# Performance work log

Hardware: AMD Instinct MI355X
Metric: run time of the kernel (lower is better)

Reference implementation:

```python
import jax, jax.numpy as jnp
import numpy as np

NUM_HEADS = 16
EMBED_DIM = 1024

def setup_inputs() -> dict:
    key = jax.random.key(0)
    k1, k2, k3 = jax.random.split(key, 3)
    x = jax.random.normal(k1, (4, 2048, EMBED_DIM), dtype=jnp.float32)
    # Linear weights (lecun-style scaling for numerical sanity)
    w_qkv = jax.random.normal(k2, (EMBED_DIM, 3 * EMBED_DIM), dtype=jnp.float32) / np.sqrt(EMBED_DIM)
    w_out = jax.random.normal(k3, (EMBED_DIM, EMBED_DIM), dtype=jnp.float32) / np.sqrt(EMBED_DIM)
    return {"x": x, "w_qkv": w_qkv, "w_out": w_out}

def reference(x, w_qkv, w_out):
    b, s, d = x.shape
    h = NUM_HEADS
    dh = d // h
    qkv = x @ w_qkv                        # [b, s, 3d]
    q, k, v = jnp.split(qkv, 3, axis=-1)   # each [b, s, d]
    def split_heads(t):
        return t.reshape(b, s, h, dh).transpose(0, 2, 1, 3)  # [b, h, s, dh]
    q, k, v = split_heads(q), split_heads(k), split_heads(v)
    logits = jnp.einsum('bhsd,bhtd->bhst', q, k) / jnp.sqrt(jnp.asarray(dh, q.dtype))
    weights = jax.nn.softmax(logits, axis=-1)
    out = jnp.einsum('bhst,bhtd->bhsd', weights, v)
    out = out.transpose(0, 2, 1, 3).reshape(b, s, d)  # [b, s, d]
    return out @ w_out
```

## Files before the change

### kernel.cpp

```cpp
#include <hip/hip_runtime.h>
#include <hip/hip_bf16.h>
#include <math.h>

typedef unsigned short u16;
typedef unsigned long long u64;
typedef __attribute__((ext_vector_type(8))) short short8;
typedef __attribute__((ext_vector_type(4))) float floatx4;

#define BB 4
#define SS 2048
#define DD 1024
#define HH 16
#define DHH 64
#define BSZ (BB*SS)

__device__ inline u16 bf1(float f) {
  return (u16)((__float_as_uint(f) + 0x8000u) >> 16);
}
__device__ inline unsigned pk2bf(float a, float b) {
  return __builtin_amdgcn_perm(__float_as_uint(b) + 0x8000u,
                               __float_as_uint(a) + 0x8000u, 0x07060302u);
}

__device__ inline short8 ld16(const u16* p) {
  union { uint4 u; short8 s; } cv;
  cv.u = *(const uint4*)p;
  return cv.s;
}

__device__ inline void gload_lds16(const u16* g, u16* l) {
  __builtin_amdgcn_global_load_lds(
      (const __attribute__((address_space(1))) void*)g,
      (__attribute__((address_space(3))) void*)l, 16, 0, 0);
}

__global__ __launch_bounds__(256) void cvt_f32_bf16(
    const float* __restrict__ in, u16* __restrict__ out) {
  int t = blockIdx.x * 256 + threadIdx.x;
  const float4* p = (const float4*)in + (size_t)t * 2;
  float4 a = p[0], b = p[1];
  uint4 r;
  r.x = pk2bf(a.x, a.y); r.y = pk2bf(a.z, a.w);
  r.z = pk2bf(b.x, b.y); r.w = pk2bf(b.z, b.w);
  *((uint4*)out + t) = r;
}

__global__ __launch_bounds__(256) void transpose_f32_bf16(
    const float* __restrict__ in, u16* __restrict__ out, int K, int N) {
  __shared__ u16 tile[32][33];
  int k0 = blockIdx.y * 32, n0 = blockIdx.x * 32;
  int tx = threadIdx.x, ty = threadIdx.y;
  #pragma unroll
  for (int i = 0; i < 32; i += 8)
    tile[ty + i][tx] = bf1(in[(size_t)(k0 + ty + i) * N + n0 + tx]);
  __syncthreads();
  #pragma unroll
  for (int i = 0; i < 32; i += 8)
    out[(size_t)(n0 + ty + i) * K + k0 + tx] = tile[tx][ty + i];
}

template <int MODE>
__global__ __launch_bounds__(256) void gemm_nt(
    const u16* __restrict__ A, const u16* __restrict__ Bt,
    int M, int N, int K,
    float* __restrict__ outf, u16* __restrict__ q, u16* __restrict__ kk,
    u16* __restrict__ vv) {
  __shared__ __attribute__((aligned(16))) u16 As[128 * 32];
  __shared__ __attribute__((aligned(16))) u16 Bs[128 * 32];
  const int tid = threadIdx.x;
  const int lane = tid & 63;
  const int wave = tid >> 6;
  const int col = lane & 15, quad = lane >> 4;
  const int m0 = blockIdx.y * 128, n0 = blockIdx.x * 128;
  const int wm = (wave & 1) * 64, wn = (wave >> 1) * 64;

  floatx4 acc[4][4];
  #pragma unroll
  for (int i = 0; i < 4; i++)
    #pragma unroll
    for (int j = 0; j < 4; j++) acc[i][j] = (floatx4){0.f, 0.f, 0.f, 0.f};

  const u16* ga0 = A + (size_t)(m0 + (tid >> 2)) * K + (tid & 3) * 8;
  const u16* ga1 = ga0 + (size_t)64 * K;
  const u16* gb0 = Bt + (size_t)(n0 + (tid >> 2)) * K + (tid & 3) * 8;
  const u16* gb1 = gb0 + (size_t)64 * K;
  u16* lA0 = As + wave * 512;
  u16* lB0 = Bs + wave * 512;

  for (int kb = 0; kb < K; kb += 32) {
    __syncthreads();
    gload_lds16(ga0 + kb, lA0);
    gload_lds16(ga1 + kb, lA0 + 2048);
    gload_lds16(gb0 + kb, lB0);
    gload_lds16(gb1 + kb, lB0 + 2048);
    __syncthreads();
    short8 af[4], bfr[4];
    #pragma unroll
    for (int i = 0; i < 4; i++)
      af[i] = ld16(As + (wm + i * 16 + col) * 32 + quad * 8);
    #pragma unroll
    for (int i = 0; i < 4; i++)
      bfr[i] = ld16(Bs + (wn + i * 16 + col) * 32 + quad * 8);
    #pragma unroll
    for (int i = 0; i < 4; i++)
      #pragma unroll
      for (int j = 0; j < 4; j++)
        acc[i][j] = __builtin_amdgcn_mfma_f32_16x16x32_bf16(af[i], bfr[j],
                                                            acc[i][j], 0, 0, 0);
  }

  #pragma unroll
  for (int i = 0; i < 4; i++) {
    #pragma unroll
    for (int j = 0; j < 4; j++) {
      int gm0 = m0 + wm + i * 16 + quad * 4;
      int gn = n0 + wn + j * 16 + col;
      if (MODE == 0) {
        #pragma unroll
        for (int r = 0; r < 4; r++)
          outf[(size_t)(gm0 + r) * N + gn] = acc[i][j][r];
      } else {
        int which = gn >> 10;
        if (which == 2) {
          int dh = gn & 63, hh = (gn >> 6) & 15;
          int bb = gm0 >> 11, s = gm0 & 2047;
          uint2 pk;
          pk.x = pk2bf(acc[i][j][0], acc[i][j][1]);
          pk.y = pk2bf(acc[i][j][2], acc[i][j][3]);
          *(uint2*)(vv + ((size_t)((bb * HH + hh) * 64 + dh)) * SS + s) = pk;
        } else {
          int f = gn & 1023;
          u16* dst = (which == 0) ? q : kk;
          float sc = (which == 0) ? 0.18033688f : 1.0f;
          #pragma unroll
          for (int r = 0; r < 4; r++)
            dst[(size_t)(gm0 + r) * DD + f] = bf1(acc[i][j][r] * sc);
        }
      }
    }
  }
}

__global__ __launch_bounds__(256) void attn_kernel(
    const u16* __restrict__ Q, const u16* __restrict__ K,
    const u16* __restrict__ VT, u16* __restrict__ O) {
  __shared__ __attribute__((aligned(16))) u16 Ks[64 * 72];
  __shared__ __attribute__((aligned(16))) u16 Vs[80 * 72];
  __shared__ __attribute__((aligned(16))) u16 Ps[4][32 * 72];

  const int tid = threadIdx.x, lane = tid & 63, wave = tid >> 6;
  const int col = lane & 15, quad = lane >> 4;
  const int idx = blockIdx.x;
  const int qt = idx & 15;
  const int h = (idx >> 4) & 15;
  const int b = idx >> 8;

  const size_t rowbase = (size_t)b * SS;
  const int qrow0 = qt * 128 + wave * 32;

  short8 qf[2][2];
  #pragma unroll
  for (int qs = 0; qs < 2; qs++)
    #pragma unroll
    for (int kc = 0; kc < 2; kc++)
      qf[qs][kc] = ld16(Q + (rowbase + qrow0 + qs * 16 + col) * DD + h * DHH +
                        kc * 32 + quad * 8);

  const u16* kg = K + rowbase * DD + h * DHH;
  const u16* vg = VT + (size_t)(b * HH + h) * DHH * SS;

  {
    int r = 64 + (tid >> 4), c = (tid & 15) * 4;
    u16 val = (r == 64) ? (u16)0x3F80 : (u16)0;
    Vs[r * 72 + c] = val; Vs[r * 72 + c + 1] = val;
    Vs[r * 72 + c + 2] = val; Vs[r * 72 + c + 3] = val;
  }

  floatx4 o[2][5];
  #pragma unroll
  for (int qs = 0; qs < 2; qs++)
    #pragma unroll
    for (int mt = 0; mt < 5; mt++) o[qs][mt] = (floatx4){0.f, 0.f, 0.f, 0.f};

  const int srow = tid >> 2, sc = (tid & 3) * 16;
  u16* pw = &Ps[wave][0];

  for (int kt = 0; kt < SS; kt += 64) {
    uint4 k0 = *(const uint4*)(kg + (size_t)(kt + srow) * DD + sc);
    uint4 k1 = *(const uint4*)(kg + (size_t)(kt + srow) * DD + sc + 8);
    uint4 v0 = *(const uint4*)(vg + (size_t)srow * SS + kt + sc);
    uint4 v1 = *(const uint4*)(vg + (size_t)srow * SS + kt + sc + 8);
    __syncthreads();
    *(uint4*)(Ks + srow * 72 + sc) = k0;
    *(uint4*)(Ks + srow * 72 + sc + 8) = k1;
    *(uint4*)(Vs + srow * 72 + sc) = v0;
    *(uint4*)(Vs + srow * 72 + sc + 8) = v1;
    __syncthreads();

    #pragma unroll
    for (int qs = 0; qs < 2; qs++) {
      #pragma unroll
      for (int mt = 0; mt < 4; mt++) {
        floatx4 s = (floatx4){0.f, 0.f, 0.f, 0.f};
        s = __builtin_amdgcn_mfma_f32_16x16x32_bf16(
            ld16(Ks + (mt * 16 + col) * 72 + quad * 8), qf[qs][0], s, 0, 0, 0);
        s = __builtin_amdgcn_mfma_f32_16x16x32_bf16(
            ld16(Ks + (mt * 16 + col) * 72 + 32 + quad * 8), qf[qs][1], s, 0, 0, 0);
        uint2 pk;
        pk.x = pk2bf(__builtin_amdgcn_exp2f(s[0]), __builtin_amdgcn_exp2f(s[1]));
        pk.y = pk2bf(__builtin_amdgcn_exp2f(s[2]), __builtin_amdgcn_exp2f(s[3]));
        *(uint2*)(pw + (qs * 16 + col) * 72 + mt * 16 + quad * 4) = pk;
      }
    }

    #pragma unroll
    for (int qs = 0; qs < 2; qs++) {
      #pragma unroll
      for (int mt = 0; mt < 5; mt++) {
        #pragma unroll
        for (int kc = 0; kc < 2; kc++) {
          short8 a = ld16(Vs + (mt * 16 + col) * 72 + kc * 32 + quad * 8);
          short8 bb = ld16(pw + (qs * 16 + col) * 72 + kc * 32 + quad * 8);
          o[qs][mt] =
              __builtin_amdgcn_mfma_f32_16x16x32_bf16(a, bb, o[qs][mt], 0, 0, 0);
        }
      }
    }
  }

  #pragma unroll
  for (int qs = 0; qs < 2; qs++) {
    float l = __shfl(o[qs][4][0], col, 64);
    float inv = 1.0f / l;
    u16* ob = O + (rowbase + qrow0 + qs * 16 + col) * DD + h * DHH;
    #pragma unroll
    for (int mt = 0; mt < 4; mt++) {
      uint2 pk;
      pk.x = pk2bf(o[qs][mt][0] * inv, o[qs][mt][1] * inv);
      pk.y = pk2bf(o[qs][mt][2] * inv, o[qs][mt][3] * inv);
      *(uint2*)(ob + mt * 16 + quad * 4) = pk;
    }
  }
}

extern "C" void kernel_launch(void* const* d_in, const int* in_sizes, int n_in,
                              void* d_out, int out_size, void* d_ws,
                              size_t ws_size, hipStream_t stream) {
  const float* x = (const float*)d_in[0];
  const float* w_qkv = (const float*)d_in[1];
  const float* w_out = (const float*)d_in[2];
  float* out = (float*)d_out;

  u16* ws = (u16*)d_ws;
  u16* wT = ws;
  u16* q = wT + (size_t)3072 * 1024;
  u16* vt = q + (size_t)BSZ * DD;
  u16* k = (u16*)d_out;
  u16* xb = k + (size_t)BSZ * DD;
  u16* att = q;

  cvt_f32_bf16<<<dim3(BSZ * DD / (256 * 8)), 256, 0, stream>>>(x, xb);
  transpose_f32_bf16<<<dim3(3072 / 32, 1024 / 32), dim3(32, 8), 0, stream>>>(
      w_qkv, wT, 1024, 3072);
  gemm_nt<1><<<dim3(3072 / 128, BSZ / 128), 256, 0, stream>>>(
      xb, wT, BSZ, 3072, 1024, nullptr, q, k, vt);
  transpose_f32_bf16<<<dim3(1024 / 32, 1024 / 32), dim3(32, 8), 0, stream>>>(
      w_out, wT, 1024, 1024);
  attn_kernel<<<dim3(BB * HH * (SS / 128)), 256, 0, stream>>>(q, k, vt, att);
  gemm_nt<0><<<dim3(1024 / 128, BSZ / 128), 256, 0, stream>>>(
      att, wT, BSZ, 1024, 1024, out, nullptr, nullptr, nullptr);
}
```

Measured before the change: 306.0 us.

## Prefetch next K/V tile into registers and hoist LDS fragment loads in attention

The attention kernel now issues global loads for the next K/V tile right after the shared-memory store, so load latency overlaps the current tile's MFMA work. Loop order is swapped so each K and V fragment is read from LDS once and reused across both query sub-tiles, and P fragments are loaded up front. Block indexing is remapped so consecutive blocks handle different batch-heads of the same query tile, and launch bounds request 4 blocks per CU. The prefetch raises register pressure, and the last iteration makes one wasted wrapped-around load.

```diff
diff --git a/kernel.cpp b/kernel.cpp
--- a/kernel.cpp
+++ b/kernel.cpp
@@ -141,7 +141,7 @@
   }
 }
 
-__global__ __launch_bounds__(256) void attn_kernel(
+__global__ __launch_bounds__(256, 4) void attn_kernel(
     const u16* __restrict__ Q, const u16* __restrict__ K,
     const u16* __restrict__ VT, u16* __restrict__ O) {
   __shared__ __attribute__((aligned(16))) u16 Ks[64 * 72];
@@ -151,9 +151,10 @@
   const int tid = threadIdx.x, lane = tid & 63, wave = tid >> 6;
   const int col = lane & 15, quad = lane >> 4;
   const int idx = blockIdx.x;
-  const int qt = idx & 15;
-  const int h = (idx >> 4) & 15;
-  const int b = idx >> 8;
+  const int qt = idx >> 6;
+  const int bh = idx & 63;
+  const int h = bh & 15;
+  const int b = bh >> 4;
 
   const size_t rowbase = (size_t)b * SS;
   const int qrow0 = qt * 128 + wave * 32;
@@ -167,7 +168,7 @@
                         kc * 32 + quad * 8);
 
   const u16* kg = K + rowbase * DD + h * DHH;
-  const u16* vg = VT + (size_t)(b * HH + h) * DHH * SS;
+  const u16* vg = VT + (size_t)bh * DHH * SS;
 
   {
     int r = 64 + (tid >> 4), c = (tid & 15) * 4;
@@ -185,11 +186,12 @@
   const int srow = tid >> 2, sc = (tid & 3) * 16;
   u16* pw = &Ps[wave][0];
 
+  uint4 k0 = *(const uint4*)(kg + (size_t)srow * DD + sc);
+  uint4 k1 = *(const uint4*)(kg + (size_t)srow * DD + sc + 8);
+  uint4 v0 = *(const uint4*)(vg + (size_t)srow * SS + sc);
+  uint4 v1 = *(const uint4*)(vg + (size_t)srow * SS + sc + 8);
+
   for (int kt = 0; kt < SS; kt += 64) {
-    uint4 k0 = *(const uint4*)(kg + (size_t)(kt + srow) * DD + sc);
-    uint4 k1 = *(const uint4*)(kg + (size_t)(kt + srow) * DD + sc + 8);
-    uint4 v0 = *(const uint4*)(vg + (size_t)srow * SS + kt + sc);
-    uint4 v1 = *(const uint4*)(vg + (size_t)srow * SS + kt + sc + 8);
     __syncthreads();
     *(uint4*)(Ks + srow * 72 + sc) = k0;
     *(uint4*)(Ks + srow * 72 + sc + 8) = k1;
@@ -197,15 +199,23 @@
     *(uint4*)(Vs + srow * 72 + sc + 8) = v1;
     __syncthreads();
 
-    #pragma unroll
-    for (int qs = 0; qs < 2; qs++) {
-      #pragma unroll
-      for (int mt = 0; mt < 4; mt++) {
+    {
+      int nt_ = (kt + 64) & (SS - 1);
+      k0 = *(const uint4*)(kg + (size_t)(nt_ + srow) * DD + sc);
+      k1 = *(const uint4*)(kg + (size_t)(nt_ + srow) * DD + sc + 8);
+      v0 = *(const uint4*)(vg + (size_t)srow * SS + nt_ + sc);
+      v1 = *(const uint4*)(vg + (size_t)srow * SS + nt_ + sc + 8);
+    }
+
+    #pragma unroll
+    for (int mt = 0; mt < 4; mt++) {
+      short8 kf0 = ld16(Ks + (mt * 16 + col) * 72 + quad * 8);
+      short8 kf1 = ld16(Ks + (mt * 16 + col) * 72 + 32 + quad * 8);
+      #pragma unroll
+      for (int qs = 0; qs < 2; qs++) {
         floatx4 s = (floatx4){0.f, 0.f, 0.f, 0.f};
-        s = __builtin_amdgcn_mfma_f32_16x16x32_bf16(
-            ld16(Ks + (mt * 16 + col) * 72 + quad * 8), qf[qs][0], s, 0, 0, 0);
-        s = __builtin_amdgcn_mfma_f32_16x16x32_bf16(
-            ld16(Ks + (mt * 16 + col) * 72 + 32 + quad * 8), qf[qs][1], s, 0, 0, 0);
+        s = __builtin_amdgcn_mfma_f32_16x16x32_bf16(kf0, qf[qs][0], s, 0, 0, 0);
+        s = __builtin_amdgcn_mfma_f32_16x16x32_bf16(kf1, qf[qs][1], s, 0, 0, 0);
         uint2 pk;
         pk.x = pk2bf(__builtin_amdgcn_exp2f(s[0]), __builtin_amdgcn_exp2f(s[1]));
         pk.y = pk2bf(__builtin_amdgcn_exp2f(s[2]), __builtin_amdgcn_exp2f(s[3]));
@@ -213,17 +223,22 @@
       }
     }
 
-    #pragma unroll
-    for (int qs = 0; qs < 2; qs++) {
-      #pragma unroll
-      for (int mt = 0; mt < 5; mt++) {
-        #pragma unroll
-        for (int kc = 0; kc < 2; kc++) {
-          short8 a = ld16(Vs + (mt * 16 + col) * 72 + kc * 32 + quad * 8);
-          short8 bb = ld16(pw + (qs * 16 + col) * 72 + kc * 32 + quad * 8);
-          o[qs][mt] =
-              __builtin_amdgcn_mfma_f32_16x16x32_bf16(a, bb, o[qs][mt], 0, 0, 0);
-        }
+    short8 pf[2][2];
+    #pragma unroll
+    for (int qs = 0; qs < 2; qs++)
+      #pragma unroll
+      for (int kc = 0; kc < 2; kc++)
+        pf[qs][kc] = ld16(pw + (qs * 16 + col) * 72 + kc * 32 + quad * 8);
+    #pragma unroll
+    for (int mt = 0; mt < 5; mt++) {
+      short8 a0 = ld16(Vs + (mt * 16 + col) * 72 + quad * 8);
+      short8 a1 = ld16(Vs + (mt * 16 + col) * 72 + 32 + quad * 8);
+      #pragma unroll
+      for (int qs = 0; qs < 2; qs++) {
+        o[qs][mt] =
+            __builtin_amdgcn_mfma_f32_16x16x32_bf16(a0, pf[qs][0], o[qs][mt], 0, 0, 0);
+        o[qs][mt] =
+            __builtin_amdgcn_mfma_f32_16x16x32_bf16(a1, pf[qs][1], o[qs][mt], 0, 0, 0);
       }
     }
   }
@@ -266,7 +281,7 @@
       xb, wT, BSZ, 3072, 1024, nullptr, q, k, vt);
   transpose_f32_bf16<<<dim3(1024 / 32, 1024 / 32), dim3(32, 8), 0, stream>>>(
       w_out, wT, 1024, 1024);
-  attn_kernel<<<dim3(BB * HH * (SS / 128)), 256, 0, stream>>>(q, k, vt, att);
+  attn_kernel<<<dim3(16 * BB * HH), 256, 0, stream>>>(q, k, vt, att);
   gemm_nt<0><<<dim3(1024 / 128, BSZ / 128), 256, 0, stream>>>(
       att, wT, BSZ, 1024, 1024, out, nullptr, nullptr, nullptr);
 }
```

Result: faster. 291.5 us (-4.7%).

## Restructure attention with 32x32 MFMA, double-buffered swizzled LDS and block remap

Applied to the files above, without the earlier changes.

The attention kernel now uses 32x32x16 bf16 MFMA tiles, with each wave handling 64 query rows (256 per block) instead of 32. K and V tiles are double-buffered in XOR-swizzled, unpadded LDS so the next tile's global load overlaps current compute. The row sum is now accumulated from the exp values through a shuffle, replacing the extra ones-row in V. The GEMMs use a 1D grid with a grouped block order to improve L2 reuse of weight tiles. The larger per-wave tile raises register pressure, and the attention grid drops to 512 blocks, which may leave CUs underused.

```diff
diff --git a/kernel.cpp b/kernel.cpp
--- a/kernel.cpp
+++ b/kernel.cpp
@@ -6,6 +6,7 @@
 typedef unsigned long long u64;
 typedef __attribute__((ext_vector_type(8))) short short8;
 typedef __attribute__((ext_vector_type(4))) float floatx4;
+typedef __attribute__((ext_vector_type(16))) float floatx16;
 
 #define BB 4
 #define SS 2048
@@ -71,7 +72,16 @@
   const int lane = tid & 63;
   const int wave = tid >> 6;
   const int col = lane & 15, quad = lane >> 4;
-  const int m0 = blockIdx.y * 128, n0 = blockIdx.x * 128;
+  int m_blk, n_blk;
+  if (MODE == 1) {
+    int x7 = blockIdx.x & 7, g = blockIdx.x >> 3;
+    n_blk = x7 + 8 * (g % 3);
+    m_blk = g / 3;
+  } else {
+    n_blk = blockIdx.x & 7;
+    m_blk = blockIdx.x >> 3;
+  }
+  const int m0 = m_blk * 128, n0 = n_blk * 128;
   const int wm = (wave & 1) * 64, wn = (wave >> 1) * 64;
 
   floatx4 acc[4][4];
@@ -141,104 +151,151 @@
   }
 }
 
-__global__ __launch_bounds__(256) void attn_kernel(
+__global__ __launch_bounds__(256, 2) void attn_kernel(
     const u16* __restrict__ Q, const u16* __restrict__ K,
     const u16* __restrict__ VT, u16* __restrict__ O) {
-  __shared__ __attribute__((aligned(16))) u16 Ks[64 * 72];
-  __shared__ __attribute__((aligned(16))) u16 Vs[80 * 72];
-  __shared__ __attribute__((aligned(16))) u16 Ps[4][32 * 72];
+  __shared__ __attribute__((aligned(16))) u16 Ks[2][64 * 64];
+  __shared__ __attribute__((aligned(16))) u16 Vs[2][64 * 64];
+  __shared__ __attribute__((aligned(16))) u16 Ps[4][64 * 64];
 
   const int tid = threadIdx.x, lane = tid & 63, wave = tid >> 6;
-  const int col = lane & 15, quad = lane >> 4;
+  const int m31 = lane & 31, h1 = lane >> 5, sw = lane & 7;
   const int idx = blockIdx.x;
-  const int qt = idx & 15;
-  const int h = (idx >> 4) & 15;
-  const int b = idx >> 8;
+  const int qt = idx >> 6;
+  const int bh = idx & 63;
+  const int h = bh & 15;
+  const int b = bh >> 4;
 
   const size_t rowbase = (size_t)b * SS;
-  const int qrow0 = qt * 128 + wave * 32;
-
-  short8 qf[2][2];
-  #pragma unroll
-  for (int qs = 0; qs < 2; qs++)
-    #pragma unroll
-    for (int kc = 0; kc < 2; kc++)
-      qf[qs][kc] = ld16(Q + (rowbase + qrow0 + qs * 16 + col) * DD + h * DHH +
-                        kc * 32 + quad * 8);
+  const int qrow0 = qt * 256 + wave * 64;
+
+  int soff[4];
+  #pragma unroll
+  for (int kc = 0; kc < 4; kc++) soff[kc] = ((kc * 2 + h1) ^ sw) * 8;
+
+  short8 qf[2][4];
+  #pragma unroll
+  for (int nb = 0; nb < 2; nb++)
+    #pragma unroll
+    for (int kc = 0; kc < 4; kc++)
+      qf[nb][kc] = ld16(Q + (rowbase + qrow0 + nb * 32 + m31) * DD + h * DHH +
+                        kc * 16 + h1 * 8);
 
   const u16* kg = K + rowbase * DD + h * DHH;
-  const u16* vg = VT + (size_t)(b * HH + h) * DHH * SS;
-
-  {
-    int r = 64 + (tid >> 4), c = (tid & 15) * 4;
-    u16 val = (r == 64) ? (u16)0x3F80 : (u16)0;
-    Vs[r * 72 + c] = val; Vs[r * 72 + c + 1] = val;
-    Vs[r * 72 + c + 2] = val; Vs[r * 72 + c + 3] = val;
-  }
-
-  floatx4 o[2][5];
-  #pragma unroll
-  for (int qs = 0; qs < 2; qs++)
-    #pragma unroll
-    for (int mt = 0; mt < 5; mt++) o[qs][mt] = (floatx4){0.f, 0.f, 0.f, 0.f};
-
-  const int srow = tid >> 2, sc = (tid & 3) * 16;
+  const u16* vg = VT + (size_t)bh * DHH * SS;
+
+  floatx16 o[2][2];
+  #pragma unroll
+  for (int mb = 0; mb < 2; mb++)
+    #pragma unroll
+    for (int nb = 0; nb < 2; nb++)
+      #pragma unroll
+      for (int e = 0; e < 16; e++) o[mb][nb][e] = 0.f;
+  float lr[2] = {0.f, 0.f};
+
+  const int srow = tid >> 2, s2 = (tid & 3) * 2;
+  const int d0 = srow * 64 + ((s2 ^ (srow & 7)) * 8);
+  const int d1 = srow * 64 + (((s2 + 1) ^ (srow & 7)) * 8);
+  const u16* kp = kg + (size_t)srow * DD + s2 * 8;
+  const u16* vp = vg + (size_t)srow * SS + s2 * 8;
+
+  uint4 k0 = *(const uint4*)kp, k1 = *(const uint4*)(kp + 8);
+  uint4 v0 = *(const uint4*)vp, v1 = *(const uint4*)(vp + 8);
+  *(uint4*)(&Ks[0][d0]) = k0; *(uint4*)(&Ks[0][d1]) = k1;
+  *(uint4*)(&Vs[0][d0]) = v0; *(uint4*)(&Vs[0][d1]) = v1;
+
   u16* pw = &Ps[wave][0];
 
-  for (int kt = 0; kt < SS; kt += 64) {
-    uint4 k0 = *(const uint4*)(kg + (size_t)(kt + srow) * DD + sc);
-    uint4 k1 = *(const uint4*)(kg + (size_t)(kt + srow) * DD + sc + 8);
-    uint4 v0 = *(const uint4*)(vg + (size_t)srow * SS + kt + sc);
-    uint4 v1 = *(const uint4*)(vg + (size_t)srow * SS + kt + sc + 8);
+  for (int it = 0; it < 32; ++it) {
+    const int cur = it & 1;
     __syncthreads();
-    *(uint4*)(Ks + srow * 72 + sc) = k0;
-    *(uint4*)(Ks + srow * 72 + sc + 8) = k1;
-    *(uint4*)(Vs + srow * 72 + sc) = v0;
-    *(uint4*)(Vs + srow * 72 + sc + 8) = v1;
-    __syncthreads();
-
-    #pragma unroll
-    for (int qs = 0; qs < 2; qs++) {
-      #pragma unroll
-      for (int mt = 0; mt < 4; mt++) {
-        floatx4 s = (floatx4){0.f, 0.f, 0.f, 0.f};
-        s = __builtin_amdgcn_mfma_f32_16x16x32_bf16(
-            ld16(Ks + (mt * 16 + col) * 72 + quad * 8), qf[qs][0], s, 0, 0, 0);
-        s = __builtin_amdgcn_mfma_f32_16x16x32_bf16(
-            ld16(Ks + (mt * 16 + col) * 72 + 32 + quad * 8), qf[qs][1], s, 0, 0, 0);
+
+    {
+      int ktn = ((it + 1) & 31) * 64;
+      k0 = *(const uint4*)(kp + (size_t)ktn * DD);
+      k1 = *(const uint4*)(kp + (size_t)ktn * DD + 8);
+      v0 = *(const uint4*)(vp + ktn);
+      v1 = *(const uint4*)(vp + ktn + 8);
+    }
+
+    const u16* kb = &Ks[cur][0];
+    const u16* vb = &Vs[cur][0];
+
+    float rs0 = 0.f, rs1 = 0.f;
+    #pragma unroll
+    for (int mb = 0; mb < 2; mb++) {
+      short8 kf[4];
+      #pragma unroll
+      for (int kc = 0; kc < 4; kc++)
+        kf[kc] = ld16(kb + (mb * 32 + m31) * 64 + soff[kc]);
+      #pragma unroll
+      for (int nb = 0; nb < 2; nb++) {
+        floatx16 s;
+        #pragma unroll
+        for (int e = 0; e < 16; e++) s[e] = 0.f;
+        #pragma unroll
+        for (int kc = 0; kc < 4; kc++)
+          s = __builtin_amdgcn_mfma_f32_32x32x16_bf16(kf[kc], qf[nb][kc], s,
+                                                      0, 0, 0);
+        float ps = 0.f;
+        u16* pr = pw + (nb * 32 + m31) * 64;
+        #pragma unroll
+        for (int g = 0; g < 4; g++) {
+          float e0 = __builtin_amdgcn_exp2f(s[g * 4 + 0]);
+          float e1 = __builtin_amdgcn_exp2f(s[g * 4 + 1]);
+          float e2 = __builtin_amdgcn_exp2f(s[g * 4 + 2]);
+          float e3 = __builtin_amdgcn_exp2f(s[g * 4 + 3]);
+          ps += (e0 + e1) + (e2 + e3);
+          uint2 pk;
+          pk.x = pk2bf(e0, e1);
+          pk.y = pk2bf(e2, e3);
+          *(uint2*)(pr + (((mb * 4 + g) ^ sw) * 8) + h1 * 4) = pk;
+        }
+        if (nb == 0) rs0 += ps; else rs1 += ps;
+      }
+    }
+    rs0 += __shfl_xor(rs0, 32, 64);
+    rs1 += __shfl_xor(rs1, 32, 64);
+    lr[0] += rs0;
+    lr[1] += rs1;
+
+    short8 pf[2][4];
+    #pragma unroll
+    for (int nb = 0; nb < 2; nb++)
+      #pragma unroll
+      for (int kc = 0; kc < 4; kc++)
+        pf[nb][kc] = ld16(pw + (nb * 32 + m31) * 64 + soff[kc]);
+    #pragma unroll
+    for (int mb = 0; mb < 2; mb++) {
+      short8 vf[4];
+      #pragma unroll
+      for (int kc = 0; kc < 4; kc++)
+        vf[kc] = ld16(vb + (mb * 32 + m31) * 64 + soff[kc]);
+      #pragma unroll
+      for (int nb = 0; nb < 2; nb++)
+        #pragma unroll
+        for (int kc = 0; kc < 4; kc++)
+          o[mb][nb] = __builtin_amdgcn_mfma_f32_32x32x16_bf16(
+              vf[kc], pf[nb][kc], o[mb][nb], 0, 0, 0);
+    }
+
+    *(uint4*)(&Ks[cur ^ 1][d0]) = k0; *(uint4*)(&Ks[cur ^ 1][d1]) = k1;
+    *(uint4*)(&Vs[cur ^ 1][d0]) = v0; *(uint4*)(&Vs[cur ^ 1][d1]) = v1;
+  }
+
+  #pragma unroll
+  for (int nb = 0; nb < 2; nb++) {
+    float inv = 1.0f / lr[nb];
+    u16* ob = O + (rowbase + qrow0 + nb * 32 + m31) * DD + h * DHH;
+    #pragma unroll
+    for (int mb = 0; mb < 2; mb++) {
+      #pragma unroll
+      for (int g = 0; g < 4; g++) {
         uint2 pk;
-        pk.x = pk2bf(__builtin_amdgcn_exp2f(s[0]), __builtin_amdgcn_exp2f(s[1]));
-        pk.y = pk2bf(__builtin_amdgcn_exp2f(s[2]), __builtin_amdgcn_exp2f(s[3]));
-        *(uint2*)(pw + (qs * 16 + col) * 72 + mt * 16 + quad * 4) = pk;
+        pk.x = pk2bf(o[mb][nb][g * 4 + 0] * inv, o[mb][nb][g * 4 + 1] * inv);
+        pk.y = pk2bf(o[mb][nb][g * 4 + 2] * inv, o[mb][nb][g * 4 + 3] * inv);
+        *(uint2*)(ob + mb * 32 + g * 8 + h1 * 4) = pk;
       }
-    }
-
-    #pragma unroll
-    for (int qs = 0; qs < 2; qs++) {
-      #pragma unroll
-      for (int mt = 0; mt < 5; mt++) {
-        #pragma unroll
-        for (int kc = 0; kc < 2; kc++) {
-          short8 a = ld16(Vs + (mt * 16 + col) * 72 + kc * 32 + quad * 8);
-          short8 bb = ld16(pw + (qs * 16 + col) * 72 + kc * 32 + quad * 8);
-          o[qs][mt] =
-              __builtin_amdgcn_mfma_f32_16x16x32_bf16(a, bb, o[qs][mt], 0, 0, 0);
-        }
-      }
-    }
-  }
-
-  #pragma unroll
-  for (int qs = 0; qs < 2; qs++) {
-    float l = __shfl(o[qs][4][0], col, 64);
-    float inv = 1.0f / l;
-    u16* ob = O + (rowbase + qrow0 + qs * 16 + col) * DD + h * DHH;
-    #pragma unroll
-    for (int mt = 0; mt < 4; mt++) {
-      uint2 pk;
-      pk.x = pk2bf(o[qs][mt][0] * inv, o[qs][mt][1] * inv);
-      pk.y = pk2bf(o[qs][mt][2] * inv, o[qs][mt][3] * inv);
-      *(uint2*)(ob + mt * 16 + quad * 4) = pk;
     }
   }
 }
@@ -262,11 +319,11 @@
   cvt_f32_bf16<<<dim3(BSZ * DD / (256 * 8)), 256, 0, stream>>>(x, xb);
   transpose_f32_bf16<<<dim3(3072 / 32, 1024 / 32), dim3(32, 8), 0, stream>>>(
       w_qkv, wT, 1024, 3072);
-  gemm_nt<1><<<dim3(3072 / 128, BSZ / 128), 256, 0, stream>>>(
+  gemm_nt<1><<<dim3(1536), 256, 0, stream>>>(
       xb, wT, BSZ, 3072, 1024, nullptr, q, k, vt);
   transpose_f32_bf16<<<dim3(1024 / 32, 1024 / 32), dim3(32, 8), 0, stream>>>(
       w_out, wT, 1024, 1024);
-  attn_kernel<<<dim3(BB * HH * (SS / 128)), 256, 0, stream>>>(q, k, vt, att);
-  gemm_nt<0><<<dim3(1024 / 128, BSZ / 128), 256, 0, stream>>>(
+  attn_kernel<<<dim3(8 * BB * HH), 256, 0, stream>>>(q, k, vt, att);
+  gemm_nt<0><<<dim3(512), 256, 0, stream>>>(
       att, wT, BSZ, 1024, 1024, out, nullptr, nullptr, nullptr);
 }
```

Measured after the change: 286.6 us. -6.3%, faster.
